# Optimization experiments

Measured on AMD Instinct MI355X. Metric: run time of the kernel, lower is better.

Reference implementation:

```python
import jax, jax.numpy as jnp
import numpy as np
import math

B, C = 512, 100000
H_PARAM = 0.333
S_PARAM = 64.0
M_PARAM = 0.4
T_ALPHA = 1.0
EPS = 1e-06


def setup_inputs() -> dict:
    key = jax.random.key(0)
    k1, k2, k3 = jax.random.split(key, 3)
    # cosine similarities in (-1, 1)
    logits = jax.random.uniform(k1, (B, C), dtype=jnp.float32, minval=-1.0, maxval=1.0)
    # embedding L2 norms: positive, roughly in a realistic range ~[5, 45]
    norms = jax.random.uniform(k2, (B, 1), dtype=jnp.float32, minval=5.0, maxval=45.0)
    labels = jax.random.randint(k3, (B,), 0, C, dtype=jnp.int64)
    return {"logits": logits, "norms": norms, "labels": labels}


def reference(logits, norms, labels):
    # t_alpha = 1.0 in training mode => batch_mean/std buffers equal the
    # current batch statistics exactly (torch.std is unbiased, ddof=1).
    cosine = jnp.clip(logits, -1.0 + EPS, 1.0 - EPS)              # [B, C]
    safe_norms = jax.lax.stop_gradient(jnp.clip(norms, 0.001, 100.0))  # [B, 1]

    mean = jnp.mean(safe_norms)
    std = jnp.std(safe_norms, ddof=1)

    margin_scaler = (safe_norms - mean) / (std + EPS) * H_PARAM   # [B, 1]
    margin_scaler = jnp.clip(margin_scaler, -1.0, 1.0)

    onehot = jax.nn.one_hot(labels, C, dtype=cosine.dtype)        # [B, C]

    g_angular = -M_PARAM * margin_scaler                          # [B, 1]
    theta = jnp.arccos(cosine)                                    # [B, C]
    theta_m = jnp.clip(theta + onehot * g_angular, EPS, math.pi - EPS)

    g_add = M_PARAM + M_PARAM * margin_scaler                     # [B, 1]
    cosine_m_final = jnp.cos(theta_m) - onehot * g_add            # [B, C]
    scaled = cosine_m_final * S_PARAM

    # mean cross-entropy over the batch
    logp = jax.nn.log_softmax(scaled, axis=-1)                    # [B, C]
    nll = -jnp.take_along_axis(logp, labels[:, None], axis=1)[:, 0]
    return jnp.mean(nll)
```

## Files before the change

kernel.cpp:

```cpp
#include <hip/hip_runtime.h>
#include <math.h>

#define B_SZ 512
#define C_SZ 100000
#define H_PARAM 0.333f
#define S_PARAM 64.0f
#define M_PARAM 0.4f
#define EPS 1e-6f
#define PI_F 3.14159265358979323846f

#define CHUNKS_PER_ROW 8
#define F4_PER_ROW (C_SZ / 4)
#define F4_PER_CHUNK (F4_PER_ROW / CHUNKS_PER_ROW)

__device__ inline float waveReduceSum(float v) {
#pragma unroll
    for (int off = 32; off > 0; off >>= 1) v += __shfl_xor(v, off, 64);
    return v;
}

__device__ inline float clip1(float x) {
    return fminf(fmaxf(x, -1.0f + EPS), 1.0f - EPS);
}

__global__ __launch_bounds__(256) void row_kernel(
    const float* __restrict__ logits,
    float* __restrict__ partial) {
    int row = blockIdx.x >> 3;
    int chunk = blockIdx.x & 7;
    const float4* lr4 = (const float4*)(logits + (size_t)row * C_SZ);
    int begin = chunk * F4_PER_CHUNK;
    int end = begin + F4_PER_CHUNK;

    float l = 0.f;
    for (int j = begin + threadIdx.x; j < end; j += 256) {
        float4 v = lr4[j];
        l += __expf(fmaf(S_PARAM, clip1(v.x), -S_PARAM));
        l += __expf(fmaf(S_PARAM, clip1(v.y), -S_PARAM));
        l += __expf(fmaf(S_PARAM, clip1(v.z), -S_PARAM));
        l += __expf(fmaf(S_PARAM, clip1(v.w), -S_PARAM));
    }

    __shared__ float shl[4];
    int wave = threadIdx.x >> 6, lane = threadIdx.x & 63;
    float wsum = waveReduceSum(l);
    if (lane == 0) shl[wave] = wsum;
    __syncthreads();
    if (threadIdx.x == 0) {
        partial[blockIdx.x] = shl[0] + shl[1] + shl[2] + shl[3];
    }
}

__global__ __launch_bounds__(512) void final_kernel(
    const float* __restrict__ norms,
    const float* __restrict__ logits,
    const int* __restrict__ labels,
    const float* __restrict__ partial,
    float* __restrict__ out) {
    __shared__ float sh[8];
    int i = threadIdx.x;
    int wave = i >> 6, lane = i & 63;

    float n = fminf(fmaxf(norms[i], 0.001f), 100.0f);
    float wsum = waveReduceSum(n);
    if (lane == 0) sh[wave] = wsum;
    __syncthreads();
    float total = 0.f;
#pragma unroll
    for (int w = 0; w < 8; ++w) total += sh[w];
    float mean = total * (1.0f / 512.0f);
    __syncthreads();

    float d = n - mean;
    float wss = waveReduceSum(d * d);
    if (lane == 0) sh[wave] = wss;
    __syncthreads();
    float tss = 0.f;
#pragma unroll
    for (int w = 0; w < 8; ++w) tss += sh[w];
    float sd = sqrtf(tss / 511.0f);
    __syncthreads();

    float ms = (n - mean) / (sd + EPS) * H_PARAM;
    ms = fminf(fmaxf(ms, -1.0f), 1.0f);
    float g_ang = -M_PARAM * ms;
    float g_add = M_PARAM + M_PARAM * ms;

    int lab = labels[i];
    float c = clip1(logits[(size_t)i * C_SZ + lab]);
    float theta = acosf(c);
    float tm = fminf(fmaxf(theta + g_ang, EPS), PI_F - EPS);
    float t = (cosf(tm) - g_add) * S_PARAM;
    float plain = __expf(S_PARAM * c - S_PARAM);

    float s = 0.f;
#pragma unroll
    for (int k = 0; k < CHUNKS_PER_ROW; ++k) s += partial[i * CHUNKS_PER_ROW + k];
    s = s - plain + __expf(t - S_PARAM);
    float v = S_PARAM + logf(s) - t;

    float vsum = waveReduceSum(v);
    if (lane == 0) sh[wave] = vsum;
    __syncthreads();
    if (i == 0) {
        float tot = 0.f;
#pragma unroll
        for (int w = 0; w < 8; ++w) tot += sh[w];
        out[0] = tot * (1.0f / 512.0f);
    }
}

extern "C" void kernel_launch(void* const* d_in, const int* in_sizes, int n_in,
                              void* d_out, int out_size, void* d_ws, size_t ws_size,
                              hipStream_t stream) {
    const float* logits = (const float*)d_in[0];
    const float* norms  = (const float*)d_in[1];
    const int*   labels = (const int*)d_in[2];
    float* out = (float*)d_out;

    float* partial = (float*)d_ws;

    row_kernel<<<B_SZ * CHUNKS_PER_ROW, 256, 0, stream>>>(logits, partial);
    final_kernel<<<1, 512, 0, stream>>>(norms, logits, labels, partial, out);
}
```

Baseline: 282.6 us.

## Move norm stats and target-logit math into row kernel, use nontemporal loads

The chunk-0 block of each row now computes the batch norm statistics, the margin-adjusted target logit and the plain-exp correction, and writes them to workspace. This takes the serial acos/cos and the dependent reductions off the single-block final kernel, whose tail latency is exposed. The main streaming loop also switches to nontemporal vector loads to cut cache pollution, and the final kernel reads the partials as float4. In exchange, every chunk-0 block repeats the full 512-element norm reduction, and the redundant work and extra syncs add some cost to those blocks.

```diff
diff --git a/kernel.cpp b/kernel.cpp
--- a/kernel.cpp
+++ b/kernel.cpp
@@ -13,6 +13,8 @@
 #define F4_PER_ROW (C_SZ / 4)
 #define F4_PER_CHUNK (F4_PER_ROW / CHUNKS_PER_ROW)
 
+typedef float nvec4 __attribute__((ext_vector_type(4)));
+
 __device__ inline float waveReduceSum(float v) {
 #pragma unroll
     for (int off = 32; off > 0; off >>= 1) v += __shfl_xor(v, off, 64);
@@ -25,78 +27,87 @@
 
 __global__ __launch_bounds__(256) void row_kernel(
     const float* __restrict__ logits,
-    float* __restrict__ partial) {
+    const float* __restrict__ norms,
+    const int* __restrict__ labels,
+    float* __restrict__ partial,
+    float* __restrict__ target,
+    float* __restrict__ plain) {
     int row = blockIdx.x >> 3;
     int chunk = blockIdx.x & 7;
-    const float4* lr4 = (const float4*)(logits + (size_t)row * C_SZ);
+    const nvec4* lr4 = (const nvec4*)(logits + (size_t)row * C_SZ);
     int begin = chunk * F4_PER_CHUNK;
     int end = begin + F4_PER_CHUNK;
 
+    __shared__ float sh[4];
+    int wave = threadIdx.x >> 6, lane = threadIdx.x & 63;
+
+    float c_raw = 0.f, g_ang = 0.f, g_add = 0.f;
+    if (chunk == 0) {
+        int lab = labels[row];
+        c_raw = logits[(size_t)row * C_SZ + lab];
+
+        float n0 = fminf(fmaxf(norms[threadIdx.x], 0.001f), 100.0f);
+        float n1 = fminf(fmaxf(norms[threadIdx.x + 256], 0.001f), 100.0f);
+
+        float wsum = waveReduceSum(n0 + n1);
+        if (lane == 0) sh[wave] = wsum;
+        __syncthreads();
+        float mean = (sh[0] + sh[1] + sh[2] + sh[3]) * (1.0f / 512.0f);
+        __syncthreads();
+
+        float d0 = n0 - mean, d1 = n1 - mean;
+        float wss = waveReduceSum(d0 * d0 + d1 * d1);
+        if (lane == 0) sh[wave] = wss;
+        __syncthreads();
+        float sd = sqrtf((sh[0] + sh[1] + sh[2] + sh[3]) / 511.0f);
+        __syncthreads();
+
+        float nr = fminf(fmaxf(norms[row], 0.001f), 100.0f);
+        float ms = (nr - mean) / (sd + EPS) * H_PARAM;
+        ms = fminf(fmaxf(ms, -1.0f), 1.0f);
+        g_ang = -M_PARAM * ms;
+        g_add = M_PARAM + M_PARAM * ms;
+    }
+
     float l = 0.f;
     for (int j = begin + threadIdx.x; j < end; j += 256) {
-        float4 v = lr4[j];
+        nvec4 v = __builtin_nontemporal_load(lr4 + j);
         l += __expf(fmaf(S_PARAM, clip1(v.x), -S_PARAM));
         l += __expf(fmaf(S_PARAM, clip1(v.y), -S_PARAM));
         l += __expf(fmaf(S_PARAM, clip1(v.z), -S_PARAM));
         l += __expf(fmaf(S_PARAM, clip1(v.w), -S_PARAM));
     }
 
-    __shared__ float shl[4];
-    int wave = threadIdx.x >> 6, lane = threadIdx.x & 63;
     float wsum = waveReduceSum(l);
-    if (lane == 0) shl[wave] = wsum;
+    if (lane == 0) sh[wave] = wsum;
     __syncthreads();
     if (threadIdx.x == 0) {
-        partial[blockIdx.x] = shl[0] + shl[1] + shl[2] + shl[3];
+        partial[blockIdx.x] = sh[0] + sh[1] + sh[2] + sh[3];
+        if (chunk == 0) {
+            float c = clip1(c_raw);
+            float theta = acosf(c);
+            float tm = fminf(fmaxf(theta + g_ang, EPS), PI_F - EPS);
+            target[row] = (cosf(tm) - g_add) * S_PARAM;
+            plain[row] = __expf(S_PARAM * c - S_PARAM);
+        }
     }
 }
 
 __global__ __launch_bounds__(512) void final_kernel(
-    const float* __restrict__ norms,
-    const float* __restrict__ logits,
-    const int* __restrict__ labels,
     const float* __restrict__ partial,
+    const float* __restrict__ target,
+    const float* __restrict__ plain,
     float* __restrict__ out) {
     __shared__ float sh[8];
     int i = threadIdx.x;
     int wave = i >> 6, lane = i & 63;
 
-    float n = fminf(fmaxf(norms[i], 0.001f), 100.0f);
-    float wsum = waveReduceSum(n);
-    if (lane == 0) sh[wave] = wsum;
-    __syncthreads();
-    float total = 0.f;
-#pragma unroll
-    for (int w = 0; w < 8; ++w) total += sh[w];
-    float mean = total * (1.0f / 512.0f);
-    __syncthreads();
+    const float4* p4 = (const float4*)(partial + i * CHUNKS_PER_ROW);
+    float4 a = p4[0], b = p4[1];
+    float s = (a.x + a.y) + (a.z + a.w) + (b.x + b.y) + (b.z + b.w);
 
-    float d = n - mean;
-    float wss = waveReduceSum(d * d);
-    if (lane == 0) sh[wave] = wss;
-    __syncthreads();
-    float tss = 0.f;
-#pragma unroll
-    for (int w = 0; w < 8; ++w) tss += sh[w];
-    float sd = sqrtf(tss / 511.0f);
-    __syncthreads();
-
-    float ms = (n - mean) / (sd + EPS) * H_PARAM;
-    ms = fminf(fmaxf(ms, -1.0f), 1.0f);
-    float g_ang = -M_PARAM * ms;
-    float g_add = M_PARAM + M_PARAM * ms;
-
-    int lab = labels[i];
-    float c = clip1(logits[(size_t)i * C_SZ + lab]);
-    float theta = acosf(c);
-    float tm = fminf(fmaxf(theta + g_ang, EPS), PI_F - EPS);
-    float t = (cosf(tm) - g_add) * S_PARAM;
-    float plain = __expf(S_PARAM * c - S_PARAM);
-
-    float s = 0.f;
-#pragma unroll
-    for (int k = 0; k < CHUNKS_PER_ROW; ++k) s += partial[i * CHUNKS_PER_ROW + k];
-    s = s - plain + __expf(t - S_PARAM);
+    float t = target[i];
+    s = s - plain[i] + __expf(t - S_PARAM);
     float v = S_PARAM + logf(s) - t;
 
     float vsum = waveReduceSum(v);
@@ -119,7 +130,10 @@
     float* out = (float*)d_out;
 
     float* partial = (float*)d_ws;
+    float* target  = partial + B_SZ * CHUNKS_PER_ROW;
+    float* plain   = target + B_SZ;
 
-    row_kernel<<<B_SZ * CHUNKS_PER_ROW, 256, 0, stream>>>(logits, partial);
-    final_kernel<<<1, 512, 0, stream>>>(norms, logits, labels, partial, out);
+    row_kernel<<<B_SZ * CHUNKS_PER_ROW, 256, 0, stream>>>(
+        logits, norms, labels, partial, target, plain);
+    final_kernel<<<1, 512, 0, stream>>>(partial, target, plain, out);
 }
```

Result: faster. 261.9 us (-7.3%).
